# Performance work log

Hardware: AMD Instinct MI355X
Metric: run time of the kernel (lower is better)

The kernel has to match this reference:

```python
import jax, jax.numpy as jnp
import numpy as np

N = 50000          # num nodes
E = 1_000_000      # num edges (no self loops by construction)
IN_CH = 128        # in_channels
HEADS = 4
OUT_CH = 16        # out_channels per head
HID = HEADS * OUT_CH  # 64
NEG_SLOPE = 0.2


def setup_inputs() -> dict:
    key = jax.random.key(0)
    k1, k2, k3, k4, k5, k6 = jax.random.split(key, 6)
    x = jax.random.normal(k1, (N, IN_CH), jnp.float32)
    # edges with guaranteed row != col (so add_self_loops == plain concat)
    row = jax.random.randint(k2, (E,), 0, N, dtype=jnp.int32)
    off = jax.random.randint(k3, (E,), 1, N, dtype=jnp.int32)
    col = (row + off) % N
    edge_index = jnp.stack([row, col], axis=0)  # [2, E]
    # xavier-uniform linear weight [HID, IN_CH] (bias=False in module)
    lim_w = float(np.sqrt(6.0 / (IN_CH + HID)))
    W = jax.random.uniform(k4, (HID, IN_CH), jnp.float32, -lim_w, lim_w)
    # xavier-uniform attention vectors [HEADS, OUT_CH]
    lim_a = float(np.sqrt(6.0 / (HEADS + OUT_CH)))
    att_src = jax.random.uniform(k5, (HEADS, OUT_CH), jnp.float32, -lim_a, lim_a)
    att_dst = jax.random.uniform(k6, (HEADS, OUT_CH), jnp.float32, -lim_a, lim_a)
    bias = jnp.zeros((HID,), jnp.float32)
    return {"x": x, "edge_index": edge_index, "W": W,
            "att_src": att_src, "att_dst": att_dst, "bias": bias}


def reference(x, edge_index, W, att_src, att_dst, bias):
    # add self loops (input edges have no self loops, so this matches torch)
    loops = jnp.arange(N, dtype=edge_index.dtype)
    ei = jnp.concatenate([edge_index, jnp.stack([loops, loops], axis=0)], axis=1)
    row, col = ei[0], ei[1]                      # [E+N]
    proj = (x @ W.T).reshape(N, HEADS, OUT_CH)   # [N, H, C]
    src = proj[row]                              # [E+N, H, C] gather
    dst = proj[col]                              # [E+N, H, C] gather
    # MX attention logits per edge per head
    logits = (jnp.einsum('ehc,hc->eh', src, att_src)
              + jnp.einsum('ehc,hc->eh', dst, att_dst))
    logits = jax.nn.leaky_relu(logits, NEG_SLOPE)            # [E+N, H]
    # segment softmax over destination node (all heads at once)
    m = jax.ops.segment_max(logits, col, num_segments=N)    # [N, H]
    e = jnp.exp(logits - m[col])
    s = jax.ops.segment_sum(e, col, num_segments=N)         # [N, H]
    w = e / s[col]                                           # [E+N, H]
    # attention-weighted scatter-add aggregation
    out = jax.ops.segment_sum(src * w[..., None], col, num_segments=N)  # [N, H, C]
    return out.reshape(N, HID) + bias
```

## Files before the change

### kernel.cpp

```cpp
#include <hip/hip_runtime.h>

#define IN_CH   128
#define HEADS   4
#define OUT_CH  16
#define HID     64
#define NEG_SLOPE 0.2f
#define LOG2E   1.44269504088896340736f

#define LDA 136

#define RB      6
#define RSZ     64
#define NRANGE  1024
#define SEG     8192
#define RWIN    2048
#define ECAP    1664
#define EPAD    (ECAP + 128)

typedef __attribute__((ext_vector_type(8))) short short8;
typedef __attribute__((ext_vector_type(4))) float float4v;

__device__ __forceinline__ unsigned short f2bf(float f) {
    unsigned int u = __float_as_uint(f);
    u += 0x7FFFu + ((u >> 16) & 1u);
    return (unsigned short)(u >> 16);
}
__device__ __forceinline__ unsigned int cvt_pk_bf16(float lo, float hi) {
    unsigned int r;
    asm("v_cvt_pk_bf16_f32 %0, %1, %2" : "=v"(r) : "v"(lo), "v"(hi));
    return r;
}
__device__ __forceinline__ void unpack2(unsigned int u, float& lo, float& hi) {
    lo = __uint_as_float(u << 16);
    hi = __uint_as_float(u & 0xffff0000u);
}

__global__ __launch_bounds__(256) void proj_bin_kernel(
    const float* __restrict__ x,
    const float* __restrict__ W,
    const float* __restrict__ att_src,
    const float* __restrict__ att_dst,
    unsigned short* __restrict__ proj,
    float* __restrict__ asrc,
    float* __restrict__ adst,
    const int* __restrict__ src,
    const int* __restrict__ dst,
    int* __restrict__ gcur,
    unsigned int* __restrict__ ebuf,
    int n_nodes, int n_edges, int nblk_proj)
{
    __shared__ __align__(16) char smraw[SEG * 4 + NRANGE * 4];

    const int tid = threadIdx.x;

    if (blockIdx.x >= nblk_proj) {
        unsigned int* eb = (unsigned int*)smraw;
        int*          lc = (int*)(smraw + SEG * 4);

        const int b = blockIdx.x - nblk_proj;
        #pragma unroll
        for (int i = tid; i < NRANGE; i += 256) lc[i] = 0;
        __syncthreads();

        const int e0  = b * SEG;
        const int e1  = min(e0 + SEG, n_edges);
        const int cnt = e1 - e0;

        for (int e = e0 + tid * 4; e < e1; e += 1024) {
            if (e + 4 <= e1) {
                const int4 s4 = *(const int4*)(src + e);
                const int4 d4 = *(const int4*)(dst + e);
                {
                    const int r = d4.x >> RB; atomicAdd(&lc[r], 1);
                    eb[e - e0 + 0] = ((unsigned int)r << 22) | ((unsigned int)(d4.x & (RSZ - 1)) << 16) | (unsigned int)s4.x;
                }
                {
                    const int r = d4.y >> RB; atomicAdd(&lc[r], 1);
                    eb[e - e0 + 1] = ((unsigned int)r << 22) | ((unsigned int)(d4.y & (RSZ - 1)) << 16) | (unsigned int)s4.y;
                }
                {
                    const int r = d4.z >> RB; atomicAdd(&lc[r], 1);
                    eb[e - e0 + 2] = ((unsigned int)r << 22) | ((unsigned int)(d4.z & (RSZ - 1)) << 16) | (unsigned int)s4.z;
                }
                {
                    const int r = d4.w >> RB; atomicAdd(&lc[r], 1);
                    eb[e - e0 + 3] = ((unsigned int)r << 22) | ((unsigned int)(d4.w & (RSZ - 1)) << 16) | (unsigned int)s4.w;
                }
            } else {
                for (int q = e; q < e1; ++q) {
                    const int d = dst[q];
                    const int r = d >> RB;
                    atomicAdd(&lc[r], 1);
                    eb[q - e0] = ((unsigned int)r << 22) | ((unsigned int)(d & (RSZ - 1)) << 16) | (unsigned int)src[q];
                }
            }
        }
        __syncthreads();

        for (int r = tid; r < NRANGE; r += 256) {
            const int c = lc[r];
            if (c) lc[r] = r * RWIN + atomicAdd(&gcur[r], c);
        }
        __syncthreads();

        for (int j = tid; j < cnt; j += 256) {
            const unsigned int p = eb[j];
            const int slot = atomicAdd(&lc[p >> 22], 1);
            ebuf[slot] = p & 0x3FFFFFu;
        }
        return;
    }

    unsigned short* As = (unsigned short*)smraw;
    unsigned short* Bs = (unsigned short*)(smraw + 64 * LDA * 2);

    const int n0 = blockIdx.x * 64;

    #pragma unroll
    for (int i = 0; i < 8; ++i) {
        int idx4 = i * 256 + tid;
        int row  = idx4 >> 5;
        int c4   = (idx4 & 31) * 4;
        float4 v = *(const float4*)(W + row * IN_CH + c4);
        uint2 o;
        o.x = cvt_pk_bf16(v.x, v.y);
        o.y = cvt_pk_bf16(v.z, v.w);
        *(uint2*)(&Bs[row * LDA + c4]) = o;
    }
    #pragma unroll
    for (int i = 0; i < 8; ++i) {
        int idx4 = i * 256 + tid;
        int row  = idx4 >> 5;
        int c4   = (idx4 & 31) * 4;
        int n    = n0 + row;
        float4 v = make_float4(0.f, 0.f, 0.f, 0.f);
        if (n < n_nodes) v = *(const float4*)(x + (size_t)n * IN_CH + c4);
        uint2 o;
        o.x = cvt_pk_bf16(v.x, v.y);
        o.y = cvt_pk_bf16(v.z, v.w);
        *(uint2*)(&As[row * LDA + c4]) = o;
    }
    __syncthreads();

    const int w    = tid >> 6;
    const int lane = tid & 63;
    const int l16  = lane & 15;
    const int quad = lane >> 4;

    float4v acc0 = {0.f,0.f,0.f,0.f};
    float4v acc1 = {0.f,0.f,0.f,0.f};
    float4v acc2 = {0.f,0.f,0.f,0.f};
    float4v acc3 = {0.f,0.f,0.f,0.f};

    const unsigned short* arow = &As[(w * 16 + l16) * LDA + quad * 8];
    const unsigned short* b0   = &Bs[( 0 + l16) * LDA + quad * 8];
    const unsigned short* b1   = &Bs[(16 + l16) * LDA + quad * 8];
    const unsigned short* b2   = &Bs[(32 + l16) * LDA + quad * 8];
    const unsigned short* b3   = &Bs[(48 + l16) * LDA + quad * 8];

    #pragma unroll
    for (int k0 = 0; k0 < IN_CH; k0 += 32) {
        short8 a  = *(const short8*)(arow + k0);
        acc0 = __builtin_amdgcn_mfma_f32_16x16x32_bf16(a, *(const short8*)(b0 + k0), acc0, 0, 0, 0);
        acc1 = __builtin_amdgcn_mfma_f32_16x16x32_bf16(a, *(const short8*)(b1 + k0), acc1, 0, 0, 0);
        acc2 = __builtin_amdgcn_mfma_f32_16x16x32_bf16(a, *(const short8*)(b2 + k0), acc2, 0, 0, 0);
        acc3 = __builtin_amdgcn_mfma_f32_16x16x32_bf16(a, *(const short8*)(b3 + k0), acc3, 0, 0, 0);
    }

    const float as0 = att_src[ 0 + l16], ad0 = att_dst[ 0 + l16];
    const float as1 = att_src[16 + l16], ad1 = att_dst[16 + l16];
    const float as2 = att_src[32 + l16], ad2 = att_dst[32 + l16];
    const float as3 = att_src[48 + l16], ad3 = att_dst[48 + l16];

    #pragma unroll
    for (int r = 0; r < 4; ++r) {
        const int n = n0 + w * 16 + quad * 4 + r;
        const bool ok = (n < n_nodes);
        float v0 = acc0[r], v1 = acc1[r], v2 = acc2[r], v3 = acc3[r];
        if (ok) {
            proj[(size_t)n * HID +  0 + l16] = f2bf(v0);
            proj[(size_t)n * HID + 16 + l16] = f2bf(v1);
            proj[(size_t)n * HID + 32 + l16] = f2bf(v2);
            proj[(size_t)n * HID + 48 + l16] = f2bf(v3);
        }
        float s0 = v0 * as0, s1 = v1 * as1, s2 = v2 * as2, s3 = v3 * as3;
        float d0 = v0 * ad0, d1 = v1 * ad1, d2 = v2 * ad2, d3 = v3 * ad3;
        #pragma unroll
        for (int off = 8; off >= 1; off >>= 1) {
            s0 += __shfl_down(s0, off, 16);
            s1 += __shfl_down(s1, off, 16);
            s2 += __shfl_down(s2, off, 16);
            s3 += __shfl_down(s3, off, 16);
            d0 += __shfl_down(d0, off, 16);
            d1 += __shfl_down(d1, off, 16);
            d2 += __shfl_down(d2, off, 16);
            d3 += __shfl_down(d3, off, 16);
        }
        if (ok && l16 == 0) {
            asrc[n * HEADS + 0] = s0 * LOG2E;
            asrc[n * HEADS + 1] = s1 * LOG2E;
            asrc[n * HEADS + 2] = s2 * LOG2E;
            asrc[n * HEADS + 3] = s3 * LOG2E;
            adst[n * HEADS + 0] = d0 * LOG2E;
            adst[n * HEADS + 1] = d1 * LOG2E;
            adst[n * HEADS + 2] = d2 * LOG2E;
            adst[n * HEADS + 3] = d3 * LOG2E;
        }
    }
}

__global__ __launch_bounds__(512) void gather_kernel(
    const unsigned short* __restrict__ proj,
    const float* __restrict__ asrc,
    const float* __restrict__ adst,
    const int* __restrict__ gcur,
    const unsigned int* __restrict__ ebuf,
    const float* __restrict__ bias,
    float* __restrict__ out,
    int n_nodes)
{
    __shared__ unsigned int csr_u[EPAD];
    __shared__ float e_s[EPAD * HEADS];
    __shared__ float adst_s[RSZ * HEADS];
    __shared__ int hist[RSZ];
    __shared__ int stt[RSZ];
    __shared__ int cur[RSZ];
    __shared__ int perm[RSZ];

    const int r    = blockIdx.x;
    const int base = r * RSZ;
    const int tid  = threadIdx.x;

    if (tid < RSZ) hist[tid] = 0;
    if (tid < RSZ * HEADS) {
        const int nd = tid >> 2;
        adst_s[tid] = (base + nd < n_nodes) ? adst[(base + nd) * HEADS + (tid & 3)] : 0.f;
    }
    __syncthreads();

    const int total = min(gcur[r], ECAP);
    const int s0 = r * RWIN;

    unsigned int ev0 = 0, ev1 = 0, ev2 = 0, ev3 = 0;
    const int j0 = tid, j1 = tid + 512, j2 = tid + 1024, j3 = tid + 1536;
    if (j0 < total) { ev0 = ebuf[s0 + j0]; atomicAdd(&hist[ev0 >> 16], 1); }
    if (j1 < total) { ev1 = ebuf[s0 + j1]; atomicAdd(&hist[ev1 >> 16], 1); }
    if (j2 < total) { ev2 = ebuf[s0 + j2]; atomicAdd(&hist[ev2 >> 16], 1); }
    if (j3 < total) { ev3 = ebuf[s0 + j3]; atomicAdd(&hist[ev3 >> 16], 1); }
    __syncthreads();

    if (tid < RSZ) {
        const int hv = hist[tid];
        int hc = hv;
        #pragma unroll
        for (int o = 1; o < 64; o <<= 1) {
            int u = __shfl_up(hc, o);
            if (tid >= o) hc += u;
        }
        stt[tid] = hc - hv;
        cur[tid] = hc - hv;
        int key = (hv << 6) | tid;
        #pragma unroll
        for (int k = 2; k <= 64; k <<= 1) {
            #pragma unroll
            for (int j = k >> 1; j > 0; j >>= 1) {
                const int pk = __shfl_xor(key, j);
                const bool keepMin = ((tid & j) == 0) == ((tid & k) == 0);
                key = keepMin ? min(key, pk) : max(key, pk);
            }
        }
        perm[tid] = key & 63;
    }
    __syncthreads();

    if (j0 < total) { const int sl = atomicAdd(&cur[ev0 >> 16], 1); csr_u[sl] = ev0; }
    if (j1 < total) { const int sl = atomicAdd(&cur[ev1 >> 16], 1); csr_u[sl] = ev1; }
    if (j2 < total) { const int sl = atomicAdd(&cur[ev2 >> 16], 1); csr_u[sl] = ev2; }
    if (j3 < total) { const int sl = atomicAdd(&cur[ev3 >> 16], 1); csr_u[sl] = ev3; }
    __syncthreads();

    const int tq = total * HEADS;
    for (int idx = tid; idx < tq; idx += 512) {
        const unsigned int u = csr_u[idx >> 2];
        const int hh  = idx & 3;
        const int sid = (int)(u & 0xffffu);
        float av = asrc[sid * HEADS + hh] + adst_s[((u >> 16) << 2) + hh];
        av = fmaxf(av, NEG_SLOPE * av);
        e_s[idx] = exp2f(av);
    }
    __syncthreads();

    const int l  = tid & 63;
    const int w  = tid >> 6;
    const int il = l & 7;
    const int g  = l >> 3;
    const int h  = il >> 1;
    const int ch = il * 8;

    const int nd = perm[w * 8 + g];
    int n = base + nd;
    const bool nok = (n < n_nodes);
    if (!nok) n = 0;

    const float4 bv0 = *(const float4*)(bias + ch);
    const float4 bv1 = *(const float4*)(bias + ch + 4);

    float zs = asrc[n * HEADS + h] + adst_s[nd * HEADS + h];
    zs = fmaxf(zs, NEG_SLOPE * zs);
    float s = exp2f(zs);
    float a0, a1, a2, a3, a4, a5, a6, a7;
    {
        const uint4 ps = *(const uint4*)(proj + (size_t)n * HID + ch);
        float p0, p1, p2, p3, p4, p5, p6, p7;
        unpack2(ps.x, p0, p1); unpack2(ps.y, p2, p3);
        unpack2(ps.z, p4, p5); unpack2(ps.w, p6, p7);
        a0 = s * p0; a1 = s * p1; a2 = s * p2; a3 = s * p3;
        a4 = s * p4; a5 = s * p5; a6 = s * p6; a7 = s * p7;
    }

    const int st  = stt[nd];
    const int deg = nok ? hist[nd] : 0;

    int m = deg;
    m = max(m, __shfl_xor(m, 8));
    m = max(m, __shfl_xor(m, 16));
    m = max(m, __shfl_xor(m, 32));
    const int kmax = __builtin_amdgcn_readfirstlane(m);

    #define STEP(K)                                                           \
    {                                                                         \
        const bool act = (K) < deg;                                           \
        const unsigned int u = csr_u[st + (K)];  \
        int sid = act ? (int)(u & 0xffffu) : 0;    \
        const uint4 pv = *(const uint4*)(proj + (size_t)sid * HID + ch);      \
        float e = e_s[(st + (K)) * HEADS + h];                                \
        e = act ? e : 0.f;                                                    \
        s += e;                                                               \
        float p0, p1, p2, p3, p4, p5, p6, p7;                                 \
        unpack2(pv.x, p0, p1); unpack2(pv.y, p2, p3);                         \
        unpack2(pv.z, p4, p5); unpack2(pv.w, p6, p7);                         \
        a0 = fmaf(e, p0, a0); a1 = fmaf(e, p1, a1);                           \
        a2 = fmaf(e, p2, a2); a3 = fmaf(e, p3, a3);                           \
        a4 = fmaf(e, p4, a4); a5 = fmaf(e, p5, a5);                           \
        a6 = fmaf(e, p6, a6); a7 = fmaf(e, p7, a7);                           \
    }

    for (int k = 0; k < kmax; k += 4) {
        STEP(k);
        STEP(k + 1);
        STEP(k + 2);
        STEP(k + 3);
    }
    #undef STEP

    if (nok) {
        const float inv = 1.0f / s;
        float4 o0, o1;
        o0.x = a0 * inv + bv0.x;
        o0.y = a1 * inv + bv0.y;
        o0.z = a2 * inv + bv0.z;
        o0.w = a3 * inv + bv0.w;
        o1.x = a4 * inv + bv1.x;
        o1.y = a5 * inv + bv1.y;
        o1.z = a6 * inv + bv1.z;
        o1.w = a7 * inv + bv1.w;
        *(float4*)(out + (size_t)n * HID + ch)     = o0;
        *(float4*)(out + (size_t)n * HID + ch + 4) = o1;
    }
}

static inline size_t align16(size_t o) { return (o + 15) & ~(size_t)15; }

extern "C" void kernel_launch(void* const* d_in, const int* in_sizes, int n_in,
                              void* d_out, int out_size, void* d_ws, size_t ws_size,
                              hipStream_t stream)
{
    const float* x       = (const float*)d_in[0];
    const int*   ei      = (const int*)d_in[1];
    const float* W       = (const float*)d_in[2];
    const float* att_src = (const float*)d_in[3];
    const float* att_dst = (const float*)d_in[4];
    const float* bias    = (const float*)d_in[5];
    float* out           = (float*)d_out;

    const int n_nodes = in_sizes[0] / IN_CH;
    const int n_edges = in_sizes[1] / 2;
    const int nproj   = (n_nodes + 63) / 64;
    const int nbin    = (n_edges + SEG - 1) / SEG;
    const int nrange  = (n_nodes + RSZ - 1) / RSZ;

    const int* src = ei;
    const int* dst = ei + n_edges;

    char* base = (char*)d_ws;
    size_t o = 0;
    unsigned short* proj = (unsigned short*)(base + o); o = align16(o + (size_t)n_nodes * HID * 2);
    float* asrc      = (float*)(base + o); o = align16(o + (size_t)n_nodes * HEADS * 4);
    float* adst      = (float*)(base + o); o = align16(o + (size_t)n_nodes * HEADS * 4);
    unsigned int* ebuf = (unsigned int*)(base + o); o = align16(o + (size_t)nrange * RWIN * 4);
    int*   gcur      = (int*)(base + o);   o = align16(o + (size_t)NRANGE * 4);

    hipMemsetAsync(gcur, 0, (size_t)NRANGE * 4, stream);

    proj_bin_kernel<<<nproj + nbin, 256, 0, stream>>>(
        x, W, att_src, att_dst, proj, asrc, adst,
        src, dst, gcur, ebuf, n_nodes, n_edges, nproj);

    gather_kernel<<<nrange, 512, 0, stream>>>(
        proj, asrc, adst, gcur, ebuf, bias, out, n_nodes);
}
```

Baseline: 123.3 us.

## Double projection tile and block size, vectorize per-edge exp, add loop tail

The fused projection/binning kernel now runs 512 threads per block, and each projection block covers 128 nodes instead of 64, so fewer blocks each reload W. The per-edge attention exponent loop now handles all four heads per edge with float4 loads and stores, replacing four scalar iterations. The aggregation unroll loop gets an exact tail so it no longer runs masked extra steps past the degree. The hidden MFMA section must correctly cover 128 rows with 8 waves; if it still assumes 64 rows the result would be wrong, and larger blocks may lower occupancy.

```diff
diff --git a/kernel.cpp b/kernel.cpp
--- a/kernel.cpp
+++ b/kernel.cpp
@@ -16,6 +16,7 @@
 #define RWIN    2048
 #define ECAP    1664
 #define EPAD    (ECAP + 128)
+#define PROJN   128
 
 typedef __attribute__((ext_vector_type(8))) short short8;
 typedef __attribute__((ext_vector_type(4))) float float4v;
@@ -35,7 +36,7 @@
     hi = __uint_as_float(u & 0xffff0000u);
 }
 
-__global__ __launch_bounds__(256) void proj_bin_kernel(
+__global__ __launch_bounds__(512) void proj_bin_kernel(
     const float* __restrict__ x,
     const float* __restrict__ W,
     const float* __restrict__ att_src,
@@ -49,7 +50,7 @@
     unsigned int* __restrict__ ebuf,
     int n_nodes, int n_edges, int nblk_proj)
 {
-    __shared__ __align__(16) char smraw[SEG * 4 + NRANGE * 4];
+    __shared__ __align__(16) char smraw[PROJN * LDA * 2 + 64 * LDA * 2];
 
     const int tid = threadIdx.x;
 
@@ -59,14 +60,14 @@
 
         const int b = blockIdx.x - nblk_proj;
         #pragma unroll
-        for (int i = tid; i < NRANGE; i += 256) lc[i] = 0;
+        for (int i = tid; i < NRANGE; i += 512) lc[i] = 0;
         __syncthreads();
 
         const int e0  = b * SEG;
         const int e1  = min(e0 + SEG, n_edges);
         const int cnt = e1 - e0;
 
-        for (int e = e0 + tid * 4; e < e1; e += 1024) {
+        for (int e = e0 + tid * 4; e < e1; e += 2048) {
             if (e + 4 <= e1) {
                 const int4 s4 = *(const int4*)(src + e);
                 const int4 d4 = *(const int4*)(dst + e);
@@ -97,13 +98,13 @@
         }
         __syncthreads();
 
-        for (int r = tid; r < NRANGE; r += 256) {
+        for (int r = tid; r < NRANGE; r += 512) {
             const int c = lc[r];
             if (c) lc[r] = r * RWIN + atomicAdd(&gcur[r], c);
         }
         __syncthreads();
 
-        for (int j = tid; j < cnt; j += 256) {
+        for (int j = tid; j < cnt; j += 512) {
             const unsigned int p = eb[j];
             const int slot = atomicAdd(&lc[p >> 22], 1);
             ebuf[slot] = p & 0x3FFFFFu;
@@ -112,13 +113,13 @@
     }
 
     unsigned short* As = (unsigned short*)smraw;
-    unsigned short* Bs = (unsigned short*)(smraw + 64 * LDA * 2);
-
-    const int n0 = blockIdx.x * 64;
+    unsigned short* Bs = (unsigned short*)(smraw + PROJN * LDA * 2);
+
+    const int n0 = blockIdx.x * PROJN;
 
     #pragma unroll
-    for (int i = 0; i < 8; ++i) {
-        int idx4 = i * 256 + tid;
+    for (int i = 0; i < 4; ++i) {
+        int idx4 = i * 512 + tid;
         int row  = idx4 >> 5;
         int c4   = (idx4 & 31) * 4;
         float4 v = *(const float4*)(W + row * IN_CH + c4);
@@ -129,7 +130,7 @@
     }
     #pragma unroll
     for (int i = 0; i < 8; ++i) {
-        int idx4 = i * 256 + tid;
+        int idx4 = i * 512 + tid;
         int row  = idx4 >> 5;
         int c4   = (idx4 & 31) * 4;
         int n    = n0 + row;
@@ -220,8 +221,8 @@
     int n_nodes)
 {
     __shared__ unsigned int csr_u[EPAD];
-    __shared__ float e_s[EPAD * HEADS];
-    __shared__ float adst_s[RSZ * HEADS];
+    __shared__ __align__(16) float e_s[EPAD * HEADS];
+    __shared__ __align__(16) float adst_s[RSZ * HEADS];
     __shared__ int hist[RSZ];
     __shared__ int stt[RSZ];
     __shared__ int cur[RSZ];
@@ -279,14 +280,19 @@
     if (j3 < total) { const int sl = atomicAdd(&cur[ev3 >> 16], 1); csr_u[sl] = ev3; }
     __syncthreads();
 
-    const int tq = total * HEADS;
-    for (int idx = tid; idx < tq; idx += 512) {
-        const unsigned int u = csr_u[idx >> 2];
-        const int hh  = idx & 3;
+    for (int j = tid; j < total; j += 512) {
+        const unsigned int u = csr_u[j];
         const int sid = (int)(u & 0xffffu);
-        float av = asrc[sid * HEADS + hh] + adst_s[((u >> 16) << 2) + hh];
-        av = fmaxf(av, NEG_SLOPE * av);
-        e_s[idx] = exp2f(av);
+        const int dl  = (int)(u >> 16);
+        const float4 s4 = *(const float4*)(asrc + sid * HEADS);
+        const float4 d4 = *(const float4*)(adst_s + dl * HEADS);
+        float4 e4;
+        float z;
+        z = s4.x + d4.x; e4.x = exp2f(fmaxf(z, NEG_SLOPE * z));
+        z = s4.y + d4.y; e4.y = exp2f(fmaxf(z, NEG_SLOPE * z));
+        z = s4.z + d4.z; e4.z = exp2f(fmaxf(z, NEG_SLOPE * z));
+        z = s4.w + d4.w; e4.w = exp2f(fmaxf(z, NEG_SLOPE * z));
+        *(float4*)(e_s + j * HEADS) = e4;
     }
     __syncthreads();
 
@@ -345,12 +351,16 @@
         a6 = fmaf(e, p6, a6); a7 = fmaf(e, p7, a7);                           \
     }
 
-    for (int k = 0; k < kmax; k += 4) {
+    const int k4 = kmax & ~3;
+    for (int k = 0; k < k4; k += 4) {
         STEP(k);
         STEP(k + 1);
         STEP(k + 2);
         STEP(k + 3);
     }
+    if (k4     < kmax) STEP(k4);
+    if (k4 + 1 < kmax) STEP(k4 + 1);
+    if (k4 + 2 < kmax) STEP(k4 + 2);
     #undef STEP
 
     if (nok) {
@@ -385,7 +395,7 @@
 
     const int n_nodes = in_sizes[0] / IN_CH;
     const int n_edges = in_sizes[1] / 2;
-    const int nproj   = (n_nodes + 63) / 64;
+    const int nproj   = (n_nodes + PROJN - 1) / PROJN;
     const int nbin    = (n_edges + SEG - 1) / SEG;
     const int nrange  = (n_nodes + RSZ - 1) / RSZ;
 
@@ -402,7 +412,7 @@
 
     hipMemsetAsync(gcur, 0, (size_t)NRANGE * 4, stream);
 
-    proj_bin_kernel<<<nproj + nbin, 256, 0, stream>>>(
+    proj_bin_kernel<<<nproj + nbin, 512, 0, stream>>>(
         x, W, att_src, att_dst, proj, asrc, adst,
         src, dst, gcur, ebuf, n_nodes, n_edges, nproj);
 
```

Result: faster. 119.0 us (-3.4%).
